# Optimization experiments

Measured on AMD Instinct MI355X. Metric: run time of the kernel, lower is better.

## Reference

```python
import jax, jax.numpy as jnp
import numpy as np

D_MODEL = 1024
N_HEADS = 16
HEAD_DIM = D_MODEL // N_HEADS
D_FF = 4096
B, T = 2, 2048
LN_EPS = 1e-5


def setup_inputs() -> dict:
    key = jax.random.key(0)
    ks = jax.random.split(key, 12)
    s = 0.02
    return {
        "x": jax.random.normal(ks[0], (B, T, D_MODEL), jnp.float32),
        "ln1_g": jnp.ones((D_MODEL,), jnp.float32),
        "ln1_b": jnp.zeros((D_MODEL,), jnp.float32),
        "w_qkv": jax.random.normal(ks[1], (D_MODEL, 3 * D_MODEL), jnp.float32) * s,
        "b_qkv": jnp.zeros((3 * D_MODEL,), jnp.float32),
        "w_out": jax.random.normal(ks[2], (D_MODEL, D_MODEL), jnp.float32) * s,
        "b_out": jnp.zeros((D_MODEL,), jnp.float32),
        "ln2_g": jnp.ones((D_MODEL,), jnp.float32),
        "ln2_b": jnp.zeros((D_MODEL,), jnp.float32),
        "w_ff1": jax.random.normal(ks[3], (D_MODEL, D_FF), jnp.float32) * s,
        "b_ff1": jnp.zeros((D_FF,), jnp.float32),
        "w_ff2": jax.random.normal(ks[4], (D_FF, D_MODEL), jnp.float32) * s,
        "b_ff2": jnp.zeros((D_MODEL,), jnp.float32),
    }


def _layernorm(x, g, b):
    mu = jnp.mean(x, axis=-1, keepdims=True)
    var = jnp.mean(jnp.square(x - mu), axis=-1, keepdims=True)
    return (x - mu) * jax.lax.rsqrt(var + LN_EPS) * g + b


def _attention(h, w_qkv, b_qkv, w_out, b_out):
    Bx, Tx, C = h.shape
    qkv = h @ w_qkv + b_qkv  # [B,T,3C]
    q, k, v = jnp.split(qkv, 3, axis=-1)
    # [B,H,T,Dh]
    q = q.reshape(Bx, Tx, N_HEADS, HEAD_DIM).transpose(0, 2, 1, 3)
    k = k.reshape(Bx, Tx, N_HEADS, HEAD_DIM).transpose(0, 2, 1, 3)
    v = v.reshape(Bx, Tx, N_HEADS, HEAD_DIM).transpose(0, 2, 1, 3)
    scale = 1.0 / np.sqrt(HEAD_DIM).astype(np.float32)
    scores = jnp.einsum("bhqd,bhkd->bhqk", q, k) * scale
    causal = jnp.tril(jnp.ones((Tx, Tx), bool))
    scores = jnp.where(causal[None, None], scores, -jnp.inf)
    attn = jax.nn.softmax(scores, axis=-1)
    out = jnp.einsum("bhqk,bhkd->bhqd", attn, v)
    out = out.transpose(0, 2, 1, 3).reshape(Bx, Tx, C)
    return out @ w_out + b_out


def reference(x, ln1_g, ln1_b, w_qkv, b_qkv, w_out, b_out,
              ln2_g, ln2_b, w_ff1, b_ff1, w_ff2, b_ff2):
    h = _layernorm(x, ln1_g, ln1_b)
    x = x + _attention(h, w_qkv, b_qkv, w_out, b_out)
    h2 = _layernorm(x, ln2_g, ln2_b)
    ff = jax.nn.relu(h2 @ w_ff1 + b_ff1) @ w_ff2 + b_ff2
    return x + ff
```

## Files before the change

kernel.cpp:

```cpp
#include <hip/hip_runtime.h>


typedef unsigned short u16;
typedef __attribute__((ext_vector_type(8))) short     bf16x8;
typedef __attribute__((ext_vector_type(4))) float     f32x4;
typedef __attribute__((ext_vector_type(8))) unsigned short u16x8;
typedef __attribute__((ext_vector_type(4))) unsigned short u16x4;

__device__ __forceinline__ u16 f2bf(float f) {
    unsigned u = __builtin_bit_cast(unsigned, f);
    unsigned r = (u + 0x7fffu + ((u >> 16) & 1u)) >> 16;
    return (u16)r;
}
__device__ __forceinline__ float bf2f(u16 h) {
    unsigned u = ((unsigned)h) << 16;
    return __builtin_bit_cast(float, u);
}
__device__ __forceinline__ f32x4 mfma16(bf16x8 a, bf16x8 b, f32x4 c) {
    return __builtin_amdgcn_mfma_f32_16x16x32_bf16(a, b, c, 0, 0, 0);
}
__device__ __forceinline__ void gl_lds16(const u16* g, u16* l) {
    __builtin_amdgcn_global_load_lds((const __attribute__((address_space(1))) void*)g,
                                     (__attribute__((address_space(3))) void*)l, 16, 0, 0);
}

__global__ __launch_bounds__(256) void wconv_kernel(const float* __restrict__ in, u16* __restrict__ out,
                                                    int R, int C) {
    __shared__ float t[32][33];
    const int tx = threadIdx.x, ty = threadIdx.y;
    const int c0 = blockIdx.x * 32, r0 = blockIdx.y * 32;
#pragma unroll
    for (int i = 0; i < 4; ++i)
        t[ty + 8 * i][tx] = in[(size_t)(r0 + ty + 8 * i) * C + c0 + tx];
    __syncthreads();
#pragma unroll
    for (int i = 0; i < 4; ++i)
        out[(size_t)(c0 + ty + 8 * i) * R + r0 + tx] = f2bf(t[tx][ty + 8 * i]);
}

__global__ __launch_bounds__(256) void ln_kernel(const float* __restrict__ x, const float* __restrict__ g,
                                                 const float* __restrict__ b, u16* __restrict__ out) {
    const int row = blockIdx.x, tid = threadIdx.x;
    const float4 v = ((const float4*)(x + (size_t)row * 1024))[tid];
    float s = v.x + v.y + v.z + v.w;
    float q = v.x * v.x + v.y * v.y + v.z * v.z + v.w * v.w;
#pragma unroll
    for (int o = 32; o; o >>= 1) { s += __shfl_xor(s, o); q += __shfl_xor(q, o); }
    __shared__ float red[8];
    if ((tid & 63) == 0) { red[(tid >> 6) * 2] = s; red[(tid >> 6) * 2 + 1] = q; }
    __syncthreads();
    s = red[0] + red[2] + red[4] + red[6];
    q = red[1] + red[3] + red[5] + red[7];
    const float mu = s * (1.0f / 1024.0f);
    const float var = q * (1.0f / 1024.0f) - mu * mu;
    const float rs = rsqrtf(var + 1e-5f);
    const float4 gv = ((const float4*)g)[tid];
    const float4 bv = ((const float4*)b)[tid];
    u16x4 o;
    o[0] = f2bf((v.x - mu) * rs * gv.x + bv.x);
    o[1] = f2bf((v.y - mu) * rs * gv.y + bv.y);
    o[2] = f2bf((v.z - mu) * rs * gv.z + bv.z);
    o[3] = f2bf((v.w - mu) * rs * gv.w + bv.w);
    ((u16x4*)(out + (size_t)row * 1024))[tid] = o;
}

template <int MODE>
__global__ __launch_bounds__(256) void gemm_kernel(const u16* __restrict__ A, const u16* __restrict__ Bt,
                                                   const float* __restrict__ bias, const float* __restrict__ resid,
                                                   void* __restrict__ Cout, int M, int N, int K) {
    __shared__ __align__(16) u16 lds[2][2][4096];
    const int tid = threadIdx.x, lane = tid & 63, wid = tid >> 6;
    const int wr = wid >> 1, wc = wid & 1, lg = lane >> 4, lc = lane & 15;
    const int m0 = blockIdx.x * 128, n0 = blockIdx.y * 128;

    const u16* ga0 = A + (size_t)(m0 + (tid >> 2)) * K + (tid & 3) * 8;
    const u16* gb0 = Bt + (size_t)(n0 + (tid >> 2)) * K + (tid & 3) * 8;

    f32x4 acc[4][4];
#pragma unroll
    for (int m = 0; m < 4; ++m)
#pragma unroll
        for (int n = 0; n < 4; ++n) acc[m][n] = (f32x4){0.f, 0.f, 0.f, 0.f};

    const int NT = K >> 5;
    auto stage = [&](int buf, int kt) {
        const u16* ga = ga0 + kt * 32;
        const u16* gb = gb0 + kt * 32;
        gl_lds16(ga, &lds[buf][0][tid * 8]);
        gl_lds16(ga + (size_t)64 * K, &lds[buf][0][2048 + tid * 8]);
        gl_lds16(gb, &lds[buf][1][tid * 8]);
        gl_lds16(gb + (size_t)64 * K, &lds[buf][1][2048 + tid * 8]);
    };
    stage(0, 0);
    for (int kt = 0; kt < NT; ++kt) {
        __syncthreads();
        if (kt + 1 < NT) stage((kt + 1) & 1, kt + 1);
        const u16* la = &lds[kt & 1][0][0];
        const u16* lb = &lds[kt & 1][1][0];
        bf16x8 a[4], bb[4];
#pragma unroll
        for (int m = 0; m < 4; ++m) a[m] = *(const bf16x8*)(la + (wr * 64 + m * 16 + lc) * 32 + lg * 8);
#pragma unroll
        for (int n = 0; n < 4; ++n) bb[n] = *(const bf16x8*)(lb + (wc * 64 + n * 16 + lc) * 32 + lg * 8);
#pragma unroll
        for (int m = 0; m < 4; ++m)
#pragma unroll
            for (int n = 0; n < 4; ++n) acc[m][n] = mfma16(a[m], bb[n], acc[m][n]);
    }
#pragma unroll
    for (int m = 0; m < 4; ++m) {
        const int row = m0 + wr * 64 + m * 16 + lg * 4;
#pragma unroll
        for (int n = 0; n < 4; ++n) {
            const int col = n0 + wc * 64 + n * 16 + lc;
            const float bv = bias[col];
#pragma unroll
            for (int r = 0; r < 4; ++r) {
                float v = acc[m][n][r] + bv;
                if (MODE == 1) v = fmaxf(v, 0.0f);
                if (MODE == 2) {
                    v += resid[(size_t)(row + r) * N + col];
                    ((float*)Cout)[(size_t)(row + r) * N + col] = v;
                } else {
                    ((u16*)Cout)[(size_t)(row + r) * N + col] = f2bf(v);
                }
            }
        }
    }
}

__global__ __launch_bounds__(256) void vtrans_kernel(const u16* __restrict__ qkv, u16* __restrict__ v_t) {
    __shared__ u16 tile[64][72];
    const int bh = blockIdx.x >> 5, tt = blockIdx.x & 31;
    const int b = bh >> 4, h = bh & 15, t0 = tt * 64;
    const int tid = threadIdx.x;
    {
        const int tl = tid >> 2, seg = (tid & 3) * 16;
        const u16* src = qkv + (size_t)(b * 2048 + t0 + tl) * 3072 + 2048 + h * 64 + seg;
        u16x8 a = *(const u16x8*)src;
        u16x8 c = *(const u16x8*)(src + 8);
#pragma unroll
        for (int j = 0; j < 8; ++j) { tile[tl][seg + j] = a[j]; tile[tl][seg + 8 + j] = c[j]; }
    }
    __syncthreads();
    {
        const int d = tid >> 2, ts = (tid & 3) * 16;
        u16x8 o0, o1;
#pragma unroll
        for (int j = 0; j < 8; ++j) { o0[j] = tile[ts + j][d]; o1[j] = tile[ts + 8 + j][d]; }
        u16* dst = v_t + ((size_t)bh * 64 + d) * 2048 + t0 + ts;
        *(u16x8*)dst = o0;
        *(u16x8*)(dst + 8) = o1;
    }
}

__global__ __launch_bounds__(256) void attn_kernel(const u16* __restrict__ qkv, const u16* __restrict__ v_t,
                                                   u16* __restrict__ attnb) {
    __shared__ __align__(16) u16 sbuf[4][64 * 68];
    const int tid = threadIdx.x, lane = tid & 63, wid = tid >> 6;
    const int lg = lane >> 4, lc = lane & 15;
    const int bh = blockIdx.x >> 3, off = blockIdx.x & 7;
    const int b = bh >> 4, h = bh & 15;
    const int qi = off + wid * 8;
    const int q0 = qi * 64;
    u16* pl = &sbuf[wid][0];

    const u16* qbase = qkv + (size_t)b * 2048 * 3072 + h * 64;
    const u16* kbase = qbase + 1024;

    bf16x8 qf[2][4];
#pragma unroll
    for (int ks = 0; ks < 2; ++ks)
#pragma unroll
        for (int nf = 0; nf < 4; ++nf)
            qf[ks][nf] = *(const bf16x8*)(qbase + (size_t)(q0 + nf * 16 + lc) * 3072 + ks * 32 + lg * 8);

    f32x4 o[4][4];
#pragma unroll
    for (int i = 0; i < 4; ++i)
#pragma unroll
        for (int j = 0; j < 4; ++j) o[i][j] = (f32x4){0.f, 0.f, 0.f, 0.f};
    float mrow[4] = {-INFINITY, -INFINITY, -INFINITY, -INFINITY};
    float lrow[4] = {0.f, 0.f, 0.f, 0.f};

    const int nkt = 2 * qi + 2;
    for (int kt = 0; kt < nkt; ++kt) {
        const int t0 = kt * 32;
        f32x4 s[2][4];
#pragma unroll
        for (int mf = 0; mf < 2; ++mf)
#pragma unroll
            for (int nf = 0; nf < 4; ++nf) s[mf][nf] = (f32x4){0.f, 0.f, 0.f, 0.f};
#pragma unroll
        for (int mf = 0; mf < 2; ++mf) {
            bf16x8 k0 = *(const bf16x8*)(kbase + (size_t)(t0 + mf * 16 + lc) * 3072 + lg * 8);
            bf16x8 k1 = *(const bf16x8*)(kbase + (size_t)(t0 + mf * 16 + lc) * 3072 + 32 + lg * 8);
#pragma unroll
            for (int nf = 0; nf < 4; ++nf) {
                s[mf][nf] = mfma16(k0, qf[0][nf], s[mf][nf]);
                s[mf][nf] = mfma16(k1, qf[1][nf], s[mf][nf]);
            }
        }
        const bool diag = (kt >= 2 * qi);
#pragma unroll
        for (int mf = 0; mf < 2; ++mf)
#pragma unroll
            for (int nf = 0; nf < 4; ++nf)
#pragma unroll
                for (int r = 0; r < 4; ++r) {
                    float v = s[mf][nf][r] * 0.125f;
                    if (diag) {
                        const int kv = t0 + mf * 16 + lg * 4 + r;
                        const int qq = q0 + nf * 16 + lc;
                        if (kv > qq) v = -INFINITY;
                    }
                    s[mf][nf][r] = v;
                }
#pragma unroll
        for (int nf = 0; nf < 4; ++nf) {
            float cm = s[0][nf][0];
#pragma unroll
            for (int mf = 0; mf < 2; ++mf)
#pragma unroll
                for (int r = 0; r < 4; ++r) cm = fmaxf(cm, s[mf][nf][r]);
            cm = fmaxf(cm, __shfl_xor(cm, 16));
            cm = fmaxf(cm, __shfl_xor(cm, 32));
            const float mn = fmaxf(mrow[nf], cm);
            const float fac = __expf(mrow[nf] - mn);
            mrow[nf] = mn;
            float cs = 0.f;
#pragma unroll
            for (int mf = 0; mf < 2; ++mf)
#pragma unroll
                for (int r = 0; r < 4; ++r) {
                    const float p = __expf(s[mf][nf][r] - mn);
                    s[mf][nf][r] = p;
                    cs += p;
                }
            cs += __shfl_xor(cs, 16);
            cs += __shfl_xor(cs, 32);
            lrow[nf] = lrow[nf] * fac + cs;
#pragma unroll
            for (int mf2 = 0; mf2 < 4; ++mf2) o[mf2][nf] *= fac;
#pragma unroll
            for (int mf = 0; mf < 2; ++mf)
#pragma unroll
                for (int r = 0; r < 4; ++r)
                    pl[(mf * 16 + lg * 4 + r) * 68 + nf * 16 + lc] = f2bf(s[mf][nf][r]);
        }
        bf16x8 pb[4];
#pragma unroll
        for (int nf = 0; nf < 4; ++nf) {
            u16x8 t;
#pragma unroll
            for (int j = 0; j < 8; ++j) t[j] = pl[(lg * 8 + j) * 68 + nf * 16 + lc];
            pb[nf] = __builtin_bit_cast(bf16x8, t);
        }
#pragma unroll
        for (int mf2 = 0; mf2 < 4; ++mf2) {
            bf16x8 vf = *(const bf16x8*)(v_t + ((size_t)bh * 64 + mf2 * 16 + lc) * 2048 + t0 + lg * 8);
#pragma unroll
            for (int nf = 0; nf < 4; ++nf) o[mf2][nf] = mfma16(vf, pb[nf], o[mf2][nf]);
        }
    }
    float inv[4];
#pragma unroll
    for (int nf = 0; nf < 4; ++nf) inv[nf] = 1.0f / lrow[nf];
    u16* ol = &sbuf[wid][0];
#pragma unroll
    for (int mf2 = 0; mf2 < 4; ++mf2)
#pragma unroll
        for (int nf = 0; nf < 4; ++nf)
#pragma unroll
            for (int r = 0; r < 4; ++r)
                ol[(mf2 * 16 + lg * 4 + r) * 68 + nf * 16 + lc] = f2bf(o[mf2][nf][r] * inv[nf]);
#pragma unroll
    for (int pass = 0; pass < 8; ++pass) {
        const int qq = pass * 8 + (lane >> 3);
        const int d0 = (lane & 7) * 8;
        u16x8 w;
#pragma unroll
        for (int j = 0; j < 8; ++j) w[j] = ol[(d0 + j) * 68 + qq];
        *(u16x8*)(attnb + (size_t)(b * 2048 + q0 + qq) * 1024 + h * 64 + d0) = w;
    }
}

extern "C" void kernel_launch(void* const* d_in, const int* in_sizes, int n_in,
                              void* d_out, int out_size, void* d_ws, size_t ws_size,
                              hipStream_t stream) {
    const float* x = (const float*)d_in[0];
    const float* ln1_g = (const float*)d_in[1];
    const float* ln1_b = (const float*)d_in[2];
    const float* w_qkv = (const float*)d_in[3];
    const float* b_qkv = (const float*)d_in[4];
    const float* w_out = (const float*)d_in[5];
    const float* b_out = (const float*)d_in[6];
    const float* ln2_g = (const float*)d_in[7];
    const float* ln2_b = (const float*)d_in[8];
    const float* w_ff1 = (const float*)d_in[9];
    const float* b_ff1 = (const float*)d_in[10];
    const float* w_ff2 = (const float*)d_in[11];
    const float* b_ff2 = (const float*)d_in[12];
    float* out = (float*)d_out;
    char* ws = (char*)d_ws;

    u16* wTqkv = (u16*)(ws + 0);
    u16* wTout = (u16*)(ws + 6291456);
    u16* wTff1 = (u16*)(ws + 8388608);
    u16* wTff2 = (u16*)(ws + 16777216);
    u16* h1    = (u16*)(ws + 25165824);
    u16* qkv   = (u16*)(ws + 33554432);
    u16* v_t   = (u16*)(ws + 58720256);
    u16* attnb = (u16*)(ws + 67108864);
    float* x2  = (float*)(ws + 75497472);
    u16* h2    = (u16*)(ws + 92274688);
    u16* ff1   = (u16*)(ws + 25165824);

    wconv_kernel<<<dim3(96, 32), dim3(32, 8), 0, stream>>>(w_qkv, wTqkv, 1024, 3072);
    wconv_kernel<<<dim3(32, 32), dim3(32, 8), 0, stream>>>(w_out, wTout, 1024, 1024);
    wconv_kernel<<<dim3(128, 32), dim3(32, 8), 0, stream>>>(w_ff1, wTff1, 1024, 4096);
    wconv_kernel<<<dim3(32, 128), dim3(32, 8), 0, stream>>>(w_ff2, wTff2, 4096, 1024);

    ln_kernel<<<4096, 256, 0, stream>>>(x, ln1_g, ln1_b, h1);
    gemm_kernel<0><<<dim3(32, 24), 256, 0, stream>>>(h1, wTqkv, b_qkv, nullptr, qkv, 4096, 3072, 1024);
    vtrans_kernel<<<1024, 256, 0, stream>>>(qkv, v_t);
    attn_kernel<<<256, 256, 0, stream>>>(qkv, v_t, attnb);
    gemm_kernel<2><<<dim3(32, 8), 256, 0, stream>>>(attnb, wTout, b_out, x, x2, 4096, 1024, 1024);
    ln_kernel<<<4096, 256, 0, stream>>>(x2, ln2_g, ln2_b, h2);
    gemm_kernel<1><<<dim3(32, 32), 256, 0, stream>>>(h2, wTff1, b_ff1, nullptr, ff1, 4096, 4096, 1024);
    gemm_kernel<2><<<dim3(32, 8), 256, 0, stream>>>(ff1, wTff2, b_ff2, x2, out, 4096, 1024, 4096);
}
```

Measured before the change: 454.2 us.

## Split causal attention KV loop across waves with LDS softmax merge

```diff
diff --git a/kernel.cpp b/kernel.cpp
--- a/kernel.cpp
+++ b/kernel.cpp
@@ -154,16 +154,17 @@
     }
 }
 
-__global__ __launch_bounds__(256) void attn_kernel(const u16* __restrict__ qkv, const u16* __restrict__ v_t,
-                                                   u16* __restrict__ attnb) {
-    __shared__ __align__(16) u16 sbuf[4][64 * 68];
+__global__ __launch_bounds__(256, 4) void attn_kernel(const u16* __restrict__ qkv, const u16* __restrict__ v_t,
+                                                      u16* __restrict__ attnb) {
+    __shared__ __align__(16) u16 wbuf[4][64 * 72];
+    __shared__ float ml[4][2][64];
     const int tid = threadIdx.x, lane = tid & 63, wid = tid >> 6;
     const int lg = lane >> 4, lc = lane & 15;
-    const int bh = blockIdx.x >> 3, off = blockIdx.x & 7;
+    const int swz = (blockIdx.x & 7) * 128 + (blockIdx.x >> 3);
+    const int qt = swz & 31, bh = swz >> 5;
     const int b = bh >> 4, h = bh & 15;
-    const int qi = off + wid * 8;
-    const int q0 = qi * 64;
-    u16* pl = &sbuf[wid][0];
+    const int q0 = qt * 64;
+    u16* pl = &wbuf[wid][0];
 
     const u16* qbase = qkv + (size_t)b * 2048 * 3072 + h * 64;
     const u16* kbase = qbase + 1024;
@@ -180,11 +181,11 @@
     for (int i = 0; i < 4; ++i)
 #pragma unroll
         for (int j = 0; j < 4; ++j) o[i][j] = (f32x4){0.f, 0.f, 0.f, 0.f};
-    float mrow[4] = {-INFINITY, -INFINITY, -INFINITY, -INFINITY};
+    float mrow[4] = {-1e30f, -1e30f, -1e30f, -1e30f};
     float lrow[4] = {0.f, 0.f, 0.f, 0.f};
 
-    const int nkt = 2 * qi + 2;
-    for (int kt = 0; kt < nkt; ++kt) {
+    const int nkt = 2 * qt + 2;
+    for (int kt = wid; kt < nkt; kt += 4) {
         const int t0 = kt * 32;
         f32x4 s[2][4];
 #pragma unroll
@@ -201,7 +202,7 @@
                 s[mf][nf] = mfma16(k1, qf[1][nf], s[mf][nf]);
             }
         }
-        const bool diag = (kt >= 2 * qi);
+        const bool diag = (kt >= 2 * qt);
 #pragma unroll
         for (int mf = 0; mf < 2; ++mf)
 #pragma unroll
@@ -212,7 +213,7 @@
                     if (diag) {
                         const int kv = t0 + mf * 16 + lg * 4 + r;
                         const int qq = q0 + nf * 16 + lc;
-                        if (kv > qq) v = -INFINITY;
+                        if (kv > qq) v = -1e30f;
                     }
                     s[mf][nf][r] = v;
                 }
@@ -243,19 +244,19 @@
 #pragma unroll
             for (int mf2 = 0; mf2 < 4; ++mf2) o[mf2][nf] *= fac;
 #pragma unroll
-            for (int mf = 0; mf < 2; ++mf)
-#pragma unroll
-                for (int r = 0; r < 4; ++r)
-                    pl[(mf * 16 + lg * 4 + r) * 68 + nf * 16 + lc] = f2bf(s[mf][nf][r]);
+            for (int mf = 0; mf < 2; ++mf) {
+                u16x4 pk;
+                pk[0] = f2bf(s[mf][nf][0]);
+                pk[1] = f2bf(s[mf][nf][1]);
+                pk[2] = f2bf(s[mf][nf][2]);
+                pk[3] = f2bf(s[mf][nf][3]);
+                *(u16x4*)(pl + (nf * 16 + lc) * 40 + mf * 16 + lg * 4) = pk;
+            }
         }
         bf16x8 pb[4];
 #pragma unroll
-        for (int nf = 0; nf < 4; ++nf) {
-            u16x8 t;
-#pragma unroll
-            for (int j = 0; j < 8; ++j) t[j] = pl[(lg * 8 + j) * 68 + nf * 16 + lc];
-            pb[nf] = __builtin_bit_cast(bf16x8, t);
-        }
+        for (int nf = 0; nf < 4; ++nf)
+            pb[nf] = *(const bf16x8*)(pl + (nf * 16 + lc) * 40 + lg * 8);
 #pragma unroll
         for (int mf2 = 0; mf2 < 4; ++mf2) {
             bf16x8 vf = *(const bf16x8*)(v_t + ((size_t)bh * 64 + mf2 * 16 + lc) * 2048 + t0 + lg * 8);
@@ -263,25 +264,49 @@
             for (int nf = 0; nf < 4; ++nf) o[mf2][nf] = mfma16(vf, pb[nf], o[mf2][nf]);
         }
     }
-    float inv[4];
-#pragma unroll
-    for (int nf = 0; nf < 4; ++nf) inv[nf] = 1.0f / lrow[nf];
-    u16* ol = &sbuf[wid][0];
+    u16* po = &wbuf[wid][0];
 #pragma unroll
     for (int mf2 = 0; mf2 < 4; ++mf2)
 #pragma unroll
-        for (int nf = 0; nf < 4; ++nf)
-#pragma unroll
-            for (int r = 0; r < 4; ++r)
-                ol[(mf2 * 16 + lg * 4 + r) * 68 + nf * 16 + lc] = f2bf(o[mf2][nf][r] * inv[nf]);
-#pragma unroll
-    for (int pass = 0; pass < 8; ++pass) {
-        const int qq = pass * 8 + (lane >> 3);
-        const int d0 = (lane & 7) * 8;
-        u16x8 w;
-#pragma unroll
-        for (int j = 0; j < 8; ++j) w[j] = ol[(d0 + j) * 68 + qq];
-        *(u16x8*)(attnb + (size_t)(b * 2048 + q0 + qq) * 1024 + h * 64 + d0) = w;
+        for (int nf = 0; nf < 4; ++nf) {
+            u16x4 pk;
+            pk[0] = f2bf(o[mf2][nf][0]);
+            pk[1] = f2bf(o[mf2][nf][1]);
+            pk[2] = f2bf(o[mf2][nf][2]);
+            pk[3] = f2bf(o[mf2][nf][3]);
+            *(u16x4*)(po + (nf * 16 + lc) * 72 + mf2 * 16 + lg * 4) = pk;
+        }
+    if (lg == 0) {
+#pragma unroll
+        for (int nf = 0; nf < 4; ++nf) {
+            ml[wid][0][nf * 16 + lc] = mrow[nf];
+            ml[wid][1][nf * 16 + lc] = lrow[nf];
+        }
+    }
+    __syncthreads();
+#pragma unroll
+    for (int rep = 0; rep < 2; ++rep) {
+        const int it = tid + rep * 256;
+        const int q = it >> 3, oc = it & 7;
+        float mv[4], lv[4];
+#pragma unroll
+        for (int w = 0; w < 4; ++w) { mv[w] = ml[w][0][q]; lv[w] = ml[w][1][q]; }
+        const float M = fmaxf(fmaxf(mv[0], mv[1]), fmaxf(mv[2], mv[3]));
+        float fw[4], L = 0.f;
+#pragma unroll
+        for (int w = 0; w < 4; ++w) { fw[w] = __expf(mv[w] - M); L += lv[w] * fw[w]; }
+        const float invL = 1.0f / L;
+        float acc[8] = {0.f, 0.f, 0.f, 0.f, 0.f, 0.f, 0.f, 0.f};
+#pragma unroll
+        for (int w = 0; w < 4; ++w) {
+            u16x8 v = *(const u16x8*)(&wbuf[w][q * 72 + oc * 8]);
+#pragma unroll
+            for (int j = 0; j < 8; ++j) acc[j] += bf2f(v[j]) * fw[w];
+        }
+        u16x8 ov;
+#pragma unroll
+        for (int j = 0; j < 8; ++j) ov[j] = f2bf(acc[j] * invL);
+        *(u16x8*)(attnb + (size_t)(b * 2048 + q0 + q) * 1024 + h * 64 + oc * 8) = ov;
     }
 }
 
@@ -324,7 +349,7 @@
     ln_kernel<<<4096, 256, 0, stream>>>(x, ln1_g, ln1_b, h1);
     gemm_kernel<0><<<dim3(32, 24), 256, 0, stream>>>(h1, wTqkv, b_qkv, nullptr, qkv, 4096, 3072, 1024);
     vtrans_kernel<<<1024, 256, 0, stream>>>(qkv, v_t);
-    attn_kernel<<<256, 256, 0, stream>>>(qkv, v_t, attnb);
+    attn_kernel<<<1024, 256, 0, stream>>>(qkv, v_t, attnb);
     gemm_kernel<2><<<dim3(32, 8), 256, 0, stream>>>(attnb, wTout, b_out, x, x2, 4096, 1024, 1024);
     ln_kernel<<<4096, 256, 0, stream>>>(x2, ln2_g, ln2_b, h2);
     gemm_kernel<1><<<dim3(32, 32), 256, 0, stream>>>(h2, wTff1, b_ff1, nullptr, ff1, 4096, 4096, 1024);
```

After: 562.8 us. 1.24x slower.
